# Kernel tuning notes

Measured on AMD Instinct MI355X. Metric: run time of the kernel, lower is better.

The kernel has to match this reference:

```python
import jax, jax.numpy as jnp
import numpy as np

BETA = 0.25
K = 1024   # num_codebook_vectors
D = 256    # latent_dim


def setup_inputs() -> dict:
    key = jax.random.key(0)
    k1, k2 = jax.random.split(key)
    z = jax.random.normal(k1, (32, D, 32, 32), dtype=jnp.float32)
    # original init: uniform(-1/K, 1/K)
    codebook = jax.random.uniform(k2, (K, D), dtype=jnp.float32, minval=-1.0 / K, maxval=1.0 / K)
    return {"z": z, "codebook": codebook}


def reference(z, codebook):
    B, C, H, W = z.shape
    sg = jax.lax.stop_gradient
    # NCHW -> NHWC, flatten to [N, D]
    z_nhwc = jnp.transpose(z, (0, 2, 3, 1))
    zf = z_nhwc.reshape(-1, C)
    # squared distances via sum-of-squares + matmul: [N, K]
    d = (jnp.sum(zf * zf, axis=1, keepdims=True)
         + jnp.sum(codebook * codebook, axis=1)
         - 2.0 * jnp.matmul(zf, codebook.T))
    idx = jnp.argmin(d, axis=1)                      # [N]
    z_q = codebook[idx].reshape(B, H, W, C)          # gather + reshape
    # commitment + codebook loss
    loss = (jnp.mean((sg(z_q) - z_nhwc) ** 2)
            + BETA * jnp.mean((z_q - sg(z_nhwc)) ** 2))
    # straight-through estimator
    z_q = z_nhwc + sg(z_q - z_nhwc)
    z_q = jnp.transpose(z_q, (0, 3, 1, 2))           # back to NCHW
    return z_q, idx, loss
```

## Files before the change

### kernel.cpp

```cpp
#include <hip/hip_runtime.h>

constexpr int D_ = 256;
constexpr int K_ = 1024;
constexpr int P_ = 1024;
constexpr int N_ = 32768;

constexpr int IDX_OFF  = 8388608;
constexpr int LOSS_OFF = 8421376;

constexpr int CB16_OFF = 0;
constexpr int CN_OFF   = 262400;
constexpr int ZN_OFF   = 263424;
constexpr int CNT_OFF  = 296448;
constexpr int WL_OFF   = 296449;

constexpr float RESCUE_MARGIN = 1e-4f;

typedef _Float16 half8 __attribute__((ext_vector_type(8)));
typedef float f32x4 __attribute__((ext_vector_type(4)));

__device__ __forceinline__ void stage16(const float* g, float* l) {
  __builtin_amdgcn_global_load_lds(
      (const __attribute__((address_space(1))) unsigned int*)g,
      (__attribute__((address_space(3))) unsigned int*)l, 16, 0, 0);
}

__global__ __launch_bounds__(64) void vq_prep(const float* __restrict__ z,
                                              const float* __restrict__ cb,
                                              float* __restrict__ scratch,
                                              float* __restrict__ loss) {
  const int blk = blockIdx.x;
  const int lane = threadIdx.x;
  if (blk < 512) {
    const int n0 = blk * 64;
    const int b = n0 >> 10, p0 = n0 & (P_ - 1);
    const float* zp = z + (size_t)b * (D_ * P_) + p0 + lane;
    float a8[8];
    #pragma unroll
    for (int i = 0; i < 8; ++i) a8[i] = 0.0f;
    for (int oct = 0; oct < 32; ++oct) {
      #pragma unroll
      for (int i = 0; i < 8; ++i) {
        float v = zp[(size_t)(oct * 8 + i) * P_];
        a8[i] = fmaf(v, v, a8[i]);
      }
    }
    scratch[ZN_OFF + n0 + lane] = ((a8[0] + a8[1]) + (a8[2] + a8[3])) +
                                  ((a8[4] + a8[5]) + (a8[6] + a8[7]));
    if (blk == 0 && lane == 0) {
      *loss = 0.0f;
      ((int*)(scratch + CNT_OFF))[0] = 0;
    }
  } else if (blk < 1536) {
    const int k = blk - 512;
    const float* row = cb + (size_t)k * D_;
    double s = 0.0;
    #pragma unroll
    for (int i = 0; i < 4; ++i) {
      double v = (double)row[lane + i * 64];
      s = fma(v, v, s);
    }
    #pragma unroll
    for (int off = 32; off; off >>= 1) s += __shfl_down(s, off, 64);
    if (lane == 0) scratch[CN_OFF + k] = (float)s;
  } else {
    const int kt = blk - 1536;
    const int k = kt * 16 + (lane & 15);
    const int quad = lane >> 4;
    _Float16* cw = (_Float16*)(scratch + CB16_OFF);
    for (int ds = 0; ds < 8; ++ds) {
      const float* src = cb + (size_t)k * D_ + ds * 32 + quad * 8;
      half8 h, lo;
      #pragma unroll
      for (int j = 0; j < 8; ++j) {
        const float v = src[j] * 1024.0f;
        const _Float16 hh = (_Float16)v;
        h[j] = hh;
        lo[j] = (_Float16)(v - (float)hh);
      }
      const int s = kt * 8 + ds;
      *(half8*)(cw + ((size_t)(s * 2 + 0) * 64 + lane) * 8) = h;
      *(half8*)(cw + ((size_t)(s * 2 + 1) * 64 + lane) * 8) = lo;
    }
  }
}

__global__ __launch_bounds__(128, 2) void vq_mfma(const float* __restrict__ z,
                                                  float* __restrict__ scratch,
                                                  float* __restrict__ idxf) {
  const int t = threadIdx.x;
  const int w = t >> 6;
  const int l = t & 63;
  const int quad = l >> 4;
  const int col = l & 15;
  const int n0 = blockIdx.x * 64;
  const int b = n0 >> 10;
  const int p0 = n0 & (P_ - 1);

  const float* __restrict__ cbsw_f = scratch + CB16_OFF;
  const float* __restrict__ cnorm = scratch + CN_OFF;
  const float* __restrict__ zn = scratch + ZN_OFF;

  __shared__ alignas(16) float Bbuf[3][4096];
  __shared__ alignas(16) float cnLds[1024];
  float* Azs = &Bbuf[2][0];

  *(float4*)(cnLds + t * 8)     = *(const float4*)(cnorm + t * 8);
  *(float4*)(cnLds + t * 8 + 4) = *(const float4*)(cnorm + t * 8 + 4);

  float znr[2][4];
  #pragma unroll
  for (int rt = 0; rt < 2; ++rt) {
    const float4 znv = *(const float4*)(zn + n0 + w * 32 + rt * 16 + quad * 4);
    znr[rt][0] = znv.x; znr[rt][1] = znv.y;
    znr[rt][2] = znv.z; znr[rt][3] = znv.w;
  }

  half8 Ah[2][8], Al[2][8];
  for (int ds = 0; ds < 8; ++ds) {
    __syncthreads();
    #pragma unroll
    for (int i = 0; i < 16; ++i) {
      const int dloc = w * 16 + i;
      Azs[l * 33 + dloc] =
          z[(size_t)b * (D_ * P_) + (size_t)(ds * 32 + dloc) * P_ + p0 + l];
    }
    __syncthreads();
    #pragma unroll
    for (int rt = 0; rt < 2; ++rt) {
      const float* src = &Azs[(w * 32 + rt * 16 + col) * 33 + quad * 8];
      half8 h, lo;
      #pragma unroll
      for (int j = 0; j < 8; ++j) {
        const float v = src[j];
        const _Float16 hh = (_Float16)v;
        h[j] = hh;
        lo[j] = (_Float16)(v - (float)hh);
      }
      Ah[rt][ds] = h;
      Al[rt][ds] = lo;
    }
  }

  asm volatile("s_waitcnt vmcnt(0)" ::: "memory");

  {
    const float* g0 = cbsw_f + l * 4;
    #pragma unroll
    for (int j = 0; j < 8; ++j) {
      const int chunk = w * 8 + j;
      stage16(g0 + chunk * 256, &Bbuf[0][chunk * 256]);
    }
    #pragma unroll
    for (int j = 0; j < 8; ++j) {
      const int chunk = w * 8 + j;
      stage16(g0 + 4096 + chunk * 256, &Bbuf[1][chunk * 256]);
    }
  }

  float m1[2][4], m2v[2][4];
  int i1[2][4];
  #pragma unroll
  for (int rt = 0; rt < 2; ++rt)
    #pragma unroll
    for (int r = 0; r < 4; ++r) { m1[rt][r] = 1e30f; m2v[rt][r] = 1e30f; i1[rt][r] = 0; }

  float* bp0 = &Bbuf[0][0];
  float* bp1 = &Bbuf[1][0];
  float* bp2 = &Bbuf[2][0];
  const float* gs = cbsw_f + 2 * 4096 + l * 4;
  const float* cnp = cnLds;
  int kg = col;

  for (int kt = 0; kt < 64; ++kt) {
    if (kt < 63) {
      asm volatile("s_waitcnt vmcnt(8)" ::: "memory");
    } else {
      asm volatile("s_waitcnt vmcnt(0)" ::: "memory");
    }
    __builtin_amdgcn_s_barrier();
    __builtin_amdgcn_sched_barrier(0);

    if (kt < 62) {
      #pragma unroll
      for (int j = 0; j < 8; ++j) {
        const int chunk = w * 8 + j;
        stage16(gs + chunk * 256, bp2 + chunk * 256);
      }
      gs += 4096;
    }

    const float cnf = cnp[col];

    f32x4 aH0 = {0.f,0.f,0.f,0.f}, aM0 = {0.f,0.f,0.f,0.f}, aL0 = {0.f,0.f,0.f,0.f};
    f32x4 aH1 = {0.f,0.f,0.f,0.f}, aM1 = {0.f,0.f,0.f,0.f}, aL1 = {0.f,0.f,0.f,0.f};

    __builtin_amdgcn_s_setprio(1);
    #pragma unroll
    for (int ds = 0; ds < 8; ++ds) {
      const half8 bh = *(const half8*)(bp0 + (ds * 2 + 0) * 256 + l * 4);
      const half8 bl = *(const half8*)(bp0 + (ds * 2 + 1) * 256 + l * 4);
      aH0 = __builtin_amdgcn_mfma_f32_16x16x32_f16(Ah[0][ds], bh, aH0, 0, 0, 0);
      aH1 = __builtin_amdgcn_mfma_f32_16x16x32_f16(Ah[1][ds], bh, aH1, 0, 0, 0);
      aM0 = __builtin_amdgcn_mfma_f32_16x16x32_f16(Ah[0][ds], bl, aM0, 0, 0, 0);
      aM1 = __builtin_amdgcn_mfma_f32_16x16x32_f16(Ah[1][ds], bl, aM1, 0, 0, 0);
      aL0 = __builtin_amdgcn_mfma_f32_16x16x32_f16(Al[0][ds], bh, aL0, 0, 0, 0);
      aL1 = __builtin_amdgcn_mfma_f32_16x16x32_f16(Al[1][ds], bh, aL1, 0, 0, 0);
    }
    __builtin_amdgcn_s_setprio(0);

    #pragma unroll
    for (int r = 0; r < 4; ++r) {
      const float s0 = fmaf((aH0[r] + aM0[r]) + aL0[r], -0x1p-9f, znr[0][r] + cnf);
      if (s0 < m1[0][r]) { m2v[0][r] = m1[0][r]; m1[0][r] = s0; i1[0][r] = kg; }
      else if (s0 < m2v[0][r]) m2v[0][r] = s0;
      const float s1 = fmaf((aH1[r] + aM1[r]) + aL1[r], -0x1p-9f, znr[1][r] + cnf);
      if (s1 < m1[1][r]) { m2v[1][r] = m1[1][r]; m1[1][r] = s1; i1[1][r] = kg; }
      else if (s1 < m2v[1][r]) m2v[1][r] = s1;
    }

    cnp += 16;
    kg += 16;
    float* tmp = bp0; bp0 = bp1; bp1 = bp2; bp2 = tmp;
  }

  #pragma unroll
  for (int off = 1; off <= 8; off <<= 1) {
    #pragma unroll
    for (int rt = 0; rt < 2; ++rt)
      #pragma unroll
      for (int r = 0; r < 4; ++r) {
        const float o1 = __shfl_xor(m1[rt][r], off, 64);
        const float o2 = __shfl_xor(m2v[rt][r], off, 64);
        const int oi = __shfl_xor(i1[rt][r], off, 64);
        if (o1 < m1[rt][r]) { m2v[rt][r] = fminf(m1[rt][r], o2); m1[rt][r] = o1; i1[rt][r] = oi; }
        else if (o1 == m1[rt][r]) { i1[rt][r] = min(i1[rt][r], oi); m2v[rt][r] = m1[rt][r]; }
        else { m2v[rt][r] = fminf(m2v[rt][r], o1); }
      }
  }

  if (col == 0) {
    int* cnt = (int*)(scratch + CNT_OFF);
    int* wl = (int*)(scratch + WL_OFF);
    #pragma unroll
    for (int rt = 0; rt < 2; ++rt)
      #pragma unroll
      for (int r = 0; r < 4; ++r) {
        const int n = n0 + w * 32 + rt * 16 + quad * 4 + r;
        idxf[n] = (float)i1[rt][r];
        if (m2v[rt][r] - m1[rt][r] < RESCUE_MARGIN) {
          const int pos = atomicAdd(cnt, 1);
          wl[pos] = n;
        }
      }
  }
}

__global__ __launch_bounds__(256, 4) void vq_rescue(const float* __restrict__ z,
                                                    const float* __restrict__ cb,
                                                    const float* __restrict__ scratch,
                                                    float* __restrict__ idxf) {
  const int tid = threadIdx.x;
  const float* cnorm = scratch + CN_OFF;
  const float* zn = scratch + ZN_OFF;
  const int count = ((const int*)(scratch + CNT_OFF))[0];
  const int* wl = (const int*)(scratch + WL_OFF);

  __shared__ alignas(16) float zb[8][D_];
  __shared__ int nrow[8];
  __shared__ float rv[256];
  __shared__ int ri[256];

  for (int base = blockIdx.x * 8; base < count; base += gridDim.x * 8) {
    const int take = min(8, count - base);
    if (tid < 8) nrow[tid] = wl[base + (tid < take ? tid : 0)];
    __syncthreads();
    #pragma unroll
    for (int r = 0; r < 8; ++r) {
      const int n = nrow[r];
      const int b = n >> 10, p = n & (P_ - 1);
      zb[r][tid] = z[(size_t)b * (D_ * P_) + (size_t)tid * P_ + p];
    }
    __syncthreads();

    const int k0 = tid * 4;
    const float4* __restrict__ cr0 = (const float4*)(cb + (size_t)(k0 + 0) * D_);
    const float4* __restrict__ cr1 = (const float4*)(cb + (size_t)(k0 + 1) * D_);
    const float4* __restrict__ cr2 = (const float4*)(cb + (size_t)(k0 + 2) * D_);
    const float4* __restrict__ cr3 = (const float4*)(cb + (size_t)(k0 + 3) * D_);

    float acc[8][4];
    #pragma unroll
    for (int r = 0; r < 8; ++r)
      #pragma unroll
      for (int j = 0; j < 4; ++j) acc[r][j] = 0.0f;

    for (int d4 = 0; d4 < 64; ++d4) {
      const float4 v0 = cr0[d4], v1 = cr1[d4], v2 = cr2[d4], v3 = cr3[d4];
      #pragma unroll
      for (int r = 0; r < 8; ++r) {
        const float4 zv = ((const float4*)zb[r])[d4];
        acc[r][0] = fmaf(zv.x, v0.x, acc[r][0]);
        acc[r][0] = fmaf(zv.y, v0.y, acc[r][0]);
        acc[r][0] = fmaf(zv.z, v0.z, acc[r][0]);
        acc[r][0] = fmaf(zv.w, v0.w, acc[r][0]);
        acc[r][1] = fmaf(zv.x, v1.x, acc[r][1]);
        acc[r][1] = fmaf(zv.y, v1.y, acc[r][1]);
        acc[r][1] = fmaf(zv.z, v1.z, acc[r][1]);
        acc[r][1] = fmaf(zv.w, v1.w, acc[r][1]);
        acc[r][2] = fmaf(zv.x, v2.x, acc[r][2]);
        acc[r][2] = fmaf(zv.y, v2.y, acc[r][2]);
        acc[r][2] = fmaf(zv.z, v2.z, acc[r][2]);
        acc[r][2] = fmaf(zv.w, v2.w, acc[r][2]);
        acc[r][3] = fmaf(zv.x, v3.x, acc[r][3]);
        acc[r][3] = fmaf(zv.y, v3.y, acc[r][3]);
        acc[r][3] = fmaf(zv.z, v3.z, acc[r][3]);
        acc[r][3] = fmaf(zv.w, v3.w, acc[r][3]);
      }
    }

    for (int r = 0; r < 8; ++r) {
      const int n = nrow[r];
      const float zA = zn[n];
      float bv = 1e30f;
      int bi = 0x7fffffff;
      #pragma unroll
      for (int j = 0; j < 4; ++j) {
        const float A = zA + cnorm[k0 + j];
        const float s = A - 2.0f * acc[r][j];
        if (s < bv) { bv = s; bi = k0 + j; }
      }
      rv[tid] = bv; ri[tid] = bi;
      __syncthreads();
      for (int off = 128; off >= 1; off >>= 1) {
        if (tid < off) {
          const float ov = rv[tid + off];
          const int oi = ri[tid + off];
          if (ov < rv[tid] || (ov == rv[tid] && oi < ri[tid])) { rv[tid] = ov; ri[tid] = oi; }
        }
        __syncthreads();
      }
      if (tid == 0 && r < take) idxf[n] = (float)ri[0];
      __syncthreads();
    }
  }
}

__global__ __launch_bounds__(256) void vq_gather(const float* __restrict__ z,
                                                 const float* __restrict__ cb,
                                                 const float* __restrict__ idxf,
                                                 float* __restrict__ out,
                                                 float* __restrict__ loss) {
  const int tid = threadIdx.x;
  const int lane = tid & 63;
  const int w = tid >> 6;
  const int n0 = blockIdx.x * 64;
  const int b = n0 >> 10;
  const int p0 = n0 & (P_ - 1);
  const int p = p0 + lane;

  const int idx = (int)(idxf[n0 + lane] + 0.5f);
  const float4* crow4 = (const float4*)(cb + (size_t)idx * D_);
  const size_t base = (size_t)b * (D_ * P_) + p;

  float acc = 0.0f;
  #pragma unroll 4
  for (int ci = 0; ci < 16; ++ci) {
    const float4 v = crow4[w * 16 + ci];
    const int c = w * 64 + ci * 4;
    const float vv[4] = {v.x, v.y, v.z, v.w};
    #pragma unroll
    for (int u = 0; u < 4; ++u) {
      const size_t a = base + (size_t)(c + u) * P_;
      const float zv = z[a];
      const float d = vv[u] - zv;
      out[a] = zv + d;
      acc = fmaf(d, d, acc);
    }
  }
  #pragma unroll
  for (int off = 32; off; off >>= 1) acc += __shfl_down(acc, off, 64);
  __shared__ float wsum[4];
  if (lane == 0) wsum[w] = acc;
  __syncthreads();
  if (tid == 0) {
    float s = wsum[0] + wsum[1] + wsum[2] + wsum[3];
    atomicAdd(loss, s * (1.25f / 8388608.0f));
  }
}

extern "C" void kernel_launch(void* const* d_in, const int* in_sizes, int n_in,
                              void* d_out, int out_size, void* d_ws, size_t ws_size,
                              hipStream_t stream) {
  const float* z = (const float*)d_in[0];
  const float* cb = (const float*)d_in[1];
  float* out = (float*)d_out;

  vq_prep<<<1600, 64, 0, stream>>>(z, cb, out, out + LOSS_OFF);
  vq_mfma<<<N_ / 64, 128, 0, stream>>>(z, out, out + IDX_OFF);
  vq_rescue<<<128, 256, 0, stream>>>(z, cb, out, out + IDX_OFF);
  vq_gather<<<N_ / 64, 256, 0, stream>>>(z, cb, out + IDX_OFF, out, out + LOSS_OFF);
}
```

Baseline: 267.5 us.

## Split codebook range across wave pairs in vq_mfma with LDS argmin merge

The MFMA distance kernel goes from 2 to 4 waves per block. Each pair of waves covers one half of the codebook, so every wave runs 32 tiles instead of 64. The triple-buffered LDS staging becomes double-buffered per half, and the top-2 results from the two halves are merged through shared memory before the index is written and rescue candidates are flagged. This aims to shorten the serial k-loop per wave and raise latency hiding, at the cost of a fully blocking vmcnt(0) wait each iteration and an extra block-wide sync and merge.

After: 226.7 us. 15.2% less time.

```diff
diff --git a/kernel.cpp b/kernel.cpp
--- a/kernel.cpp
+++ b/kernel.cpp
@@ -85,7 +85,7 @@
   }
 }
 
-__global__ __launch_bounds__(128, 2) void vq_mfma(const float* __restrict__ z,
+__global__ __launch_bounds__(256, 2) void vq_mfma(const float* __restrict__ z,
                                                   float* __restrict__ scratch,
                                                   float* __restrict__ idxf) {
   const int t = threadIdx.x;
@@ -93,6 +93,8 @@
   const int l = t & 63;
   const int quad = l >> 4;
   const int col = l & 15;
+  const int rh = w & 1;
+  const int cs = w >> 1;
   const int n0 = blockIdx.x * 64;
   const int b = n0 >> 10;
   const int p0 = n0 & (P_ - 1);
@@ -101,34 +103,37 @@
   const float* __restrict__ cnorm = scratch + CN_OFF;
   const float* __restrict__ zn = scratch + ZN_OFF;
 
-  __shared__ alignas(16) float Bbuf[3][4096];
+  __shared__ alignas(16) float Bbuf[2][2][4096];
   __shared__ alignas(16) float cnLds[1024];
-  float* Azs = &Bbuf[2][0];
-
-  *(float4*)(cnLds + t * 8)     = *(const float4*)(cnorm + t * 8);
-  *(float4*)(cnLds + t * 8 + 4) = *(const float4*)(cnorm + t * 8 + 4);
+  __shared__ float sM1[4][32];
+  __shared__ float sM2[4][32];
+  __shared__ int   sI1[4][32];
+  float* Azs = &Bbuf[0][1][0];
+
+  *(float4*)(cnLds + t * 4) = *(const float4*)(cnorm + t * 4);
 
   float znr[2][4];
   #pragma unroll
   for (int rt = 0; rt < 2; ++rt) {
-    const float4 znv = *(const float4*)(zn + n0 + w * 32 + rt * 16 + quad * 4);
+    const float4 znv = *(const float4*)(zn + n0 + rh * 32 + rt * 16 + quad * 4);
     znr[rt][0] = znv.x; znr[rt][1] = znv.y;
     znr[rt][2] = znv.z; znr[rt][3] = znv.w;
   }
 
   half8 Ah[2][8], Al[2][8];
+  const int dl0 = w * 8;
   for (int ds = 0; ds < 8; ++ds) {
     __syncthreads();
     #pragma unroll
-    for (int i = 0; i < 16; ++i) {
-      const int dloc = w * 16 + i;
+    for (int i = 0; i < 8; ++i) {
+      const int dloc = dl0 + i;
       Azs[l * 33 + dloc] =
           z[(size_t)b * (D_ * P_) + (size_t)(ds * 32 + dloc) * P_ + p0 + l];
     }
     __syncthreads();
     #pragma unroll
     for (int rt = 0; rt < 2; ++rt) {
-      const float* src = &Azs[(w * 32 + rt * 16 + col) * 33 + quad * 8];
+      const float* src = &Azs[(rh * 32 + rt * 16 + col) * 33 + quad * 8];
       half8 h, lo;
       #pragma unroll
       for (int j = 0; j < 8; ++j) {
@@ -144,18 +149,12 @@
 
   asm volatile("s_waitcnt vmcnt(0)" ::: "memory");
 
-  {
-    const float* g0 = cbsw_f + l * 4;
-    #pragma unroll
-    for (int j = 0; j < 8; ++j) {
-      const int chunk = w * 8 + j;
-      stage16(g0 + chunk * 256, &Bbuf[0][chunk * 256]);
-    }
-    #pragma unroll
-    for (int j = 0; j < 8; ++j) {
-      const int chunk = w * 8 + j;
-      stage16(g0 + 4096 + chunk * 256, &Bbuf[1][chunk * 256]);
-    }
+  const int ch0 = rh * 8;
+  const float* gsbase = cbsw_f + (size_t)cs * 32 * 4096 + l * 4;
+  #pragma unroll
+  for (int j = 0; j < 8; ++j) {
+    const int chunk = ch0 + j;
+    stage16(gsbase + chunk * 256, &Bbuf[cs][0][chunk * 256]);
   }
 
   float m1[2][4], m2v[2][4];
@@ -165,32 +164,26 @@
     #pragma unroll
     for (int r = 0; r < 4; ++r) { m1[rt][r] = 1e30f; m2v[rt][r] = 1e30f; i1[rt][r] = 0; }
 
-  float* bp0 = &Bbuf[0][0];
-  float* bp1 = &Bbuf[1][0];
-  float* bp2 = &Bbuf[2][0];
-  const float* gs = cbsw_f + 2 * 4096 + l * 4;
-  const float* cnp = cnLds;
-  int kg = col;
-
-  for (int kt = 0; kt < 64; ++kt) {
-    if (kt < 63) {
-      asm volatile("s_waitcnt vmcnt(8)" ::: "memory");
-    } else {
-      asm volatile("s_waitcnt vmcnt(0)" ::: "memory");
-    }
+  float* bcur = &Bbuf[cs][0][0];
+  float* bnxt = &Bbuf[cs][1][0];
+  const float* cnp = cnLds + cs * 512 + col;
+  int kg = cs * 512 + col;
+
+  for (int p = 0; p < 32; ++p) {
+    asm volatile("s_waitcnt vmcnt(0)" ::: "memory");
     __builtin_amdgcn_s_barrier();
     __builtin_amdgcn_sched_barrier(0);
 
-    if (kt < 62) {
+    if (p < 31) {
+      const float* gsp = gsbase + (size_t)(p + 1) * 4096;
       #pragma unroll
       for (int j = 0; j < 8; ++j) {
-        const int chunk = w * 8 + j;
-        stage16(gs + chunk * 256, bp2 + chunk * 256);
-      }
-      gs += 4096;
-    }
-
-    const float cnf = cnp[col];
+        const int chunk = ch0 + j;
+        stage16(gsp + chunk * 256, bnxt + chunk * 256);
+      }
+    }
+
+    const float cnf = *cnp;
 
     f32x4 aH0 = {0.f,0.f,0.f,0.f}, aM0 = {0.f,0.f,0.f,0.f}, aL0 = {0.f,0.f,0.f,0.f};
     f32x4 aH1 = {0.f,0.f,0.f,0.f}, aM1 = {0.f,0.f,0.f,0.f}, aL1 = {0.f,0.f,0.f,0.f};
@@ -198,8 +191,8 @@
     __builtin_amdgcn_s_setprio(1);
     #pragma unroll
     for (int ds = 0; ds < 8; ++ds) {
-      const half8 bh = *(const half8*)(bp0 + (ds * 2 + 0) * 256 + l * 4);
-      const half8 bl = *(const half8*)(bp0 + (ds * 2 + 1) * 256 + l * 4);
+      const half8 bh = *(const half8*)(bcur + (ds * 2 + 0) * 256 + l * 4);
+      const half8 bl = *(const half8*)(bcur + (ds * 2 + 1) * 256 + l * 4);
       aH0 = __builtin_amdgcn_mfma_f32_16x16x32_f16(Ah[0][ds], bh, aH0, 0, 0, 0);
       aH1 = __builtin_amdgcn_mfma_f32_16x16x32_f16(Ah[1][ds], bh, aH1, 0, 0, 0);
       aM0 = __builtin_amdgcn_mfma_f32_16x16x32_f16(Ah[0][ds], bl, aM0, 0, 0, 0);
@@ -221,7 +214,7 @@
 
     cnp += 16;
     kg += 16;
-    float* tmp = bp0; bp0 = bp1; bp1 = bp2; bp2 = tmp;
+    float* tmp = bcur; bcur = bnxt; bnxt = tmp;
   }
 
   #pragma unroll
@@ -240,15 +233,35 @@
   }
 
   if (col == 0) {
+    #pragma unroll
+    for (int rt = 0; rt < 2; ++rt)
+      #pragma unroll
+      for (int r = 0; r < 4; ++r) {
+        const int rl = rt * 16 + quad * 4 + r;
+        sM1[w][rl] = m1[rt][r];
+        sM2[w][rl] = m2v[rt][r];
+        sI1[w][rl] = i1[rt][r];
+      }
+  }
+  __syncthreads();
+  if (w < 2 && col == 0) {
     int* cnt = (int*)(scratch + CNT_OFF);
     int* wl = (int*)(scratch + WL_OFF);
     #pragma unroll
     for (int rt = 0; rt < 2; ++rt)
       #pragma unroll
       for (int r = 0; r < 4; ++r) {
-        const int n = n0 + w * 32 + rt * 16 + quad * 4 + r;
-        idxf[n] = (float)i1[rt][r];
-        if (m2v[rt][r] - m1[rt][r] < RESCUE_MARGIN) {
+        const int rl = rt * 16 + quad * 4 + r;
+        float a1 = sM1[w][rl], a2 = sM2[w][rl];
+        int ai = sI1[w][rl];
+        const float o1 = sM1[w + 2][rl], o2 = sM2[w + 2][rl];
+        const int oi = sI1[w + 2][rl];
+        if (o1 < a1) { a2 = fminf(a1, o2); a1 = o1; ai = oi; }
+        else if (o1 == a1) { ai = min(ai, oi); a2 = a1; }
+        else { a2 = fminf(a2, o1); }
+        const int n = n0 + w * 32 + rl;
+        idxf[n] = (float)ai;
+        if (a2 - a1 < RESCUE_MARGIN) {
           const int pos = atomicAdd(cnt, 1);
           wl[pos] = n;
         }
@@ -397,7 +410,7 @@
   float* out = (float*)d_out;
 
   vq_prep<<<1600, 64, 0, stream>>>(z, cb, out, out + LOSS_OFF);
-  vq_mfma<<<N_ / 64, 128, 0, stream>>>(z, out, out + IDX_OFF);
+  vq_mfma<<<N_ / 64, 256, 0, stream>>>(z, out, out + IDX_OFF);
   vq_rescue<<<128, 256, 0, stream>>>(z, cb, out, out + IDX_OFF);
   vq_gather<<<N_ / 64, 256, 0, stream>>>(z, cb, out + IDX_OFF, out, out + LOSS_OFF);
 }
```
